# Performance work log

Hardware: AMD Instinct MI355X
Metric: run time of the kernel (lower is better)

The kernel has to match this reference:

```python
import jax, jax.numpy as jnp
import numpy as np

B, N, C_IN, C_H, C_OUT, R, X_DIM = 32, 256, 64, 128, 128, 5, 1024
NEG = -9e15

def _leaky(x, s=0.2):
    return jnp.where(x >= 0, x, s * x)

def gat_layer(atoms, mask, W, b, a):
    # atoms: (B,n,c_in), mask: (B,n,n,R) bool, W: (c_in, R*c), b: (R*c,), a: (R, 2c)
    bs, n, _ = atoms.shape
    c = a.shape[1] // 2
    h = (atoms @ W + b).reshape(bs, n, R, c)            # (B,n,R,c)
    src = jnp.einsum('bnrc,rc->bnr', h, a[:, :c])       # a . h_i part
    dst = jnp.einsum('bnrc,rc->bnr', h, a[:, c:])       # a . h_j part
    logits = _leaky(src[:, :, None, :] + dst[:, None, :, :])  # (B,i,j,R)
    masked = jnp.where(mask, logits, NEG)
    probs = jax.nn.softmax(masked.reshape(bs, n, n * R), axis=2).reshape(bs, n, n, R)
    return jnp.einsum('bijr,bjrc->bic', probs, h)       # (B,n,c)

def setup_inputs() -> dict:
    key = jax.random.key(0)
    ks = jax.random.split(key, 16)
    def p(k, shape, fan):
        return jax.random.normal(k, shape, jnp.float32) * (1.414 / np.sqrt(fan))
    inp = {
        'x': jax.random.normal(ks[0], (B, X_DIM), jnp.float32),
        'y_atoms': jax.random.normal(ks[1], (B, N, C_IN), jnp.float32),
        'y_bonds': jax.random.randint(ks[2], (B, N, N, R), 0, 2, jnp.int32),
        'W1': p(ks[3], (C_IN, R * C_H), C_IN), 'b1': jnp.zeros((R * C_H,), jnp.float32),
        'a1': p(ks[4], (R, 2 * C_H), 2 * C_H),
        'W2': p(ks[5], (C_H, R * C_H), C_H), 'b2': jnp.zeros((R * C_H,), jnp.float32),
        'a2': p(ks[6], (R, 2 * C_H), 2 * C_H),
        'W3': p(ks[7], (C_H, R * C_OUT), C_H), 'b3': jnp.zeros((R * C_OUT,), jnp.float32),
        'a3': p(ks[8], (R, 2 * C_OUT), 2 * C_OUT),
        'We1': p(ks[9], (2 * C_OUT + X_DIM, 256), 2 * C_OUT + X_DIM), 'be1': jnp.zeros((256,), jnp.float32),
        'We2': p(ks[10], (256, 32), 256), 'be2': jnp.zeros((32,), jnp.float32),
        'We3': p(ks[11], (32, 1), 32), 'be3': jnp.zeros((1,), jnp.float32),
    }
    return inp

def reference(x, y_atoms, y_bonds, W1, b1, a1, W2, b2, a2, W3, b3, a3,
              We1, be1, We2, be2, We3, be3):
    mask = (y_bonds == 1)
    h = gat_layer(y_atoms, mask, W1, b1, a1)
    h = _leaky(h)                                   # dropout is identity at eval
    h = gat_layer(h, mask, W2, b2, a2)
    h = _leaky(h)
    h = gat_layer(h, mask, W3, b3, a3)
    y_feats = jnp.concatenate([jnp.mean(h, axis=1), jnp.max(h, axis=1)], axis=1)
    z = jnp.concatenate([x, y_feats], axis=1)
    z = _leaky(z @ We1 + be1)
    z = _leaky(z @ We2 + be2)
    return z @ We3 + be3
```

## Files before the change

### kernel.cpp

```cpp
#include <hip/hip_runtime.h>
#include <cstddef>

#define BB 32
#define NN 256
#define RR 5

typedef __attribute__((ext_vector_type(8))) short bf16x8;
typedef __attribute__((ext_vector_type(4))) float f32x4;

__device__ __forceinline__ float lrelu(float x) { return x >= 0.f ? x : 0.2f * x; }
__device__ __forceinline__ unsigned short f2bf(float x) {
    unsigned u = __float_as_uint(x);
    u += 0x7FFFu + ((u >> 16) & 1u);
    return (unsigned short)(u >> 16);
}
__device__ __forceinline__ float bf2f(unsigned short u) {
    return __uint_as_float((unsigned)u << 16);
}

__global__ __launch_bounds__(256) void k_prep(const float* __restrict__ W1,
                                              const float* __restrict__ W2,
                                              const float* __restrict__ W3,
                                              const float* __restrict__ We1,
                                              const int* __restrict__ bonds,
                                              unsigned short* __restrict__ WT1,
                                              unsigned short* __restrict__ WT2,
                                              unsigned short* __restrict__ WT3,
                                              float* __restrict__ We1T,
                                              unsigned char* __restrict__ maskp) {
    __shared__ float Ls[40][256];
    int blk = blockIdx.x;
    int t = threadIdx.x;
    if (blk < 30) {
        int layer = blk / 10, nt = blk % 10;
        const float* W;
        unsigned short* WT;
        int K;
        if (layer == 0)      { W = W1; WT = WT1; K = 64; }
        else if (layer == 1) { W = W2; WT = WT2; K = 128; }
        else                 { W = W3; WT = WT3; K = 128; }
        int n = nt * 64 + (t & 63);
        for (int kg = (int)(t >> 6); kg < K / 8; kg += 4) {
            bf16x8 v;
#pragma unroll
            for (int e = 0; e < 8; ++e) v[e] = (short)f2bf(W[(size_t)(kg * 8 + e) * 640 + n]);
            *(bf16x8*)&WT[(size_t)n * K + kg * 8] = v;
        }
    } else if (blk < 62) {
        int bt = blk - 30;
        for (int kk = 0; kk < 40; ++kk)
            Ls[kk][t] = We1[(size_t)(bt * 40 + kk) * 256 + t];
        __syncthreads();
#pragma unroll
        for (int q = 0; q < 10; ++q) {
            float4 v;
            v.x = Ls[q * 4 + 0][t]; v.y = Ls[q * 4 + 1][t];
            v.z = Ls[q * 4 + 2][t]; v.w = Ls[q * 4 + 3][t];
            *(float4*)&We1T[(size_t)t * 1280 + bt * 40 + q * 4] = v;
        }
    } else {
        int idx = (blk - 62) * 256 + t;
        const int* p = bonds + (size_t)idx * 5;
        unsigned m = 0;
#pragma unroll
        for (int r = 0; r < 5; ++r) m |= (p[r] == 1) ? (1u << r) : 0u;
        maskp[idx] = (unsigned char)m;
    }
}

template <int K, int MODE>
__global__ __launch_bounds__(256) void k_gemm_h(const float* __restrict__ Af32,
                                                const unsigned short* __restrict__ aggPb,
                                                const float* __restrict__ Zpart,
                                                const unsigned short* __restrict__ WTg,
                                                const float* __restrict__ bias,
                                                const float* __restrict__ avec,
                                                float* __restrict__ srcp,
                                                float* __restrict__ dstp,
                                                unsigned short* __restrict__ hTf) {
    const int t = threadIdx.x;
    const int n0 = blockIdx.x * 64, m0 = blockIdx.y * 64;
    const int w = t >> 6, lane = t & 63;
    const int colg = lane & 15, rquad = lane >> 4;
    const int m = m0 + w * 16 + colg;
    const int koff = rquad * 8;

    float zi = 0.f;
    if (MODE == 1) zi = 1.f / (Zpart[m] + Zpart[8192 + m]);

    f32x4 acc[4] = {};
#pragma unroll
    for (int kk = 0; kk < K; kk += 32) {
        bf16x8 af;
        size_t off = (size_t)m * K + kk + koff;
        if (MODE == 1) {
            bf16x8 p0 = *(const bf16x8*)&aggPb[off];
            bf16x8 p1 = *(const bf16x8*)&aggPb[off + 1048576];
#pragma unroll
            for (int e = 0; e < 8; ++e) {
                float v = bf2f((unsigned short)p0[e]) + bf2f((unsigned short)p1[e]);
                af[e] = (short)f2bf(lrelu(v * zi));
            }
        } else {
            float4 q0 = *(const float4*)&Af32[off];
            float4 q1 = *(const float4*)&Af32[off + 4];
            af[0] = (short)f2bf(q0.x); af[1] = (short)f2bf(q0.y);
            af[2] = (short)f2bf(q0.z); af[3] = (short)f2bf(q0.w);
            af[4] = (short)f2bf(q1.x); af[5] = (short)f2bf(q1.y);
            af[6] = (short)f2bf(q1.z); af[7] = (short)f2bf(q1.w);
        }
#pragma unroll
        for (int ct = 0; ct < 4; ++ct) {
            bf16x8 bfv = *(const bf16x8*)&WTg[(size_t)(n0 + ct * 16 + colg) * K + kk + koff];
            acc[ct] = __builtin_amdgcn_mfma_f32_16x16x32_bf16(af, bfv, acc[ct], 0, 0, 0);
        }
    }

    const int r = n0 >> 7, chalf = n0 & 127;
    const int b = m0 >> 8, jb = m0 & 255;
    float val[4][4];
    float ssum[4] = {0.f, 0.f, 0.f, 0.f}, dsum[4] = {0.f, 0.f, 0.f, 0.f};
#pragma unroll
    for (int ct = 0; ct < 4; ++ct) {
        int cg = chalf + ct * 16 + colg;
        float bv = bias[n0 + ct * 16 + colg];
        float asr = avec[r * 256 + cg];
        float ads = avec[r * 256 + 128 + cg];
#pragma unroll
        for (int reg = 0; reg < 4; ++reg) {
            float v = acc[ct][reg] + bv;
            val[ct][reg] = v;
            ssum[reg] += v * asr;
            dsum[reg] += v * ads;
        }
    }
#pragma unroll
    for (int mk = 1; mk < 16; mk <<= 1)
#pragma unroll
        for (int reg = 0; reg < 4; ++reg) {
            ssum[reg] += __shfl_xor(ssum[reg], mk);
            dsum[reg] += __shfl_xor(dsum[reg], mk);
        }
    if (colg == 0) {
        int half = (n0 >> 6) & 1;
#pragma unroll
        for (int reg = 0; reg < 4; ++reg) {
            int row = m0 + w * 16 + rquad * 4 + reg;
            srcp[half * 40960 + row * 5 + r] = ssum[reg];
            dstp[half * 40960 + row * 5 + r] = dsum[reg];
        }
    }
    {
        const int joct = (jb >> 3) + w * 2 + (rquad >> 1);
        const size_t tile = (size_t)((b * 5 + r) * 32 + joct) * 1024;
        const int sub = (rquad & 1) * 4;
#pragma unroll
        for (int ct = 0; ct < 4; ++ct) {
            int c = chalf + ct * 16 + colg;
            uint2 pk;
            pk.x = (unsigned)f2bf(val[ct][0]) | ((unsigned)f2bf(val[ct][1]) << 16);
            pk.y = (unsigned)f2bf(val[ct][2]) | ((unsigned)f2bf(val[ct][3]) << 16);
            *(uint2*)&hTf[tile + (size_t)c * 8 + sub] = pk;
        }
    }
}

__global__ __launch_bounds__(256) void k_agg(const unsigned short* __restrict__ hTf,
                                             const float* __restrict__ srcp,
                                             const float* __restrict__ dstp,
                                             const unsigned char* __restrict__ maskp,
                                             unsigned short* __restrict__ aggPb,
                                             float* __restrict__ Zpart) {
    __shared__ unsigned short Ps[10240];
    __shared__ float Ss[80], Ds2l[640], Zrow[16];
    const int t = threadIdx.x;
    const int js = blockIdx.x, itile = blockIdx.y, b = blockIdx.z;
    const int ib = b * 256 + itile * 16;
    const int w = t >> 6, lane = t & 63;
    const int colg = lane & 15, rquad = lane >> 4;
    const size_t bbase = (size_t)(b * 5) * 32 * 1024;

    if (t < 80) Ss[t] = srcp[(size_t)ib * 5 + t] + srcp[40960 + (size_t)ib * 5 + t];
    if (t >= 80 && t < 96) Zrow[t - 80] = 0.f;
    for (int idx = t; idx < 640; idx += 256) {
        int jl = idx & 127, rr = idx >> 7;
        size_t o = (size_t)(b * 256 + js * 128 + jl) * 5 + rr;
        Ds2l[rr * 128 + jl] = dstp[o] + dstp[40960 + o];
    }

    bf16x8 pre[2][2];
#pragma unroll
    for (int s = 0; s < 2; ++s) {
        const int joct = js * 16 + s * 4 + rquad;
        const size_t tbase = bbase + (size_t)joct * 1024;
#pragma unroll
        for (int ct = 0; ct < 2; ++ct) {
            int c = w * 32 + ct * 16 + colg;
            pre[s][ct] = *(const bf16x8*)&hTf[tbase + (size_t)c * 8];
        }
    }
    __syncthreads();

    {
        const int i = t & 15;
        float esum = 0.f;
#pragma unroll
        for (int it = 0; it < 5; ++it) {
            int p = it * 256 + t;
            int lane8 = p & 63, s = p >> 6;
            int kq = lane8 >> 4;
            int k0 = s * 32 + kq * 8;
            int rr = k0 >> 7, j0l = k0 & 127;
            uint2 mk8 = *(const uint2*)&maskp[((size_t)(ib + i) << 8) + js * 128 + j0l];
            float sv = Ss[i * 5 + rr];
            bf16x8 pv;
#pragma unroll
            for (int e = 0; e < 8; ++e) {
                unsigned mb = ((e < 4 ? (mk8.x >> (8 * e)) : (mk8.y >> (8 * (e - 4)))) >> rr) & 1u;
                float v = lrelu(sv + Ds2l[rr * 128 + j0l + e]);
                float ev = mb ? __expf(v) : 0.f;
                unsigned short q = f2bf(ev);
                pv[e] = (short)q;
                esum += __uint_as_float((unsigned)q << 16);
            }
            *(bf16x8*)&Ps[p * 8] = pv;
        }
        atomicAdd(&Zrow[i], esum);
    }
    __syncthreads();
    if (t < 16) Zpart[(size_t)js * 8192 + ib + t] = Zrow[t];

    f32x4 acc[2] = {};
#pragma unroll
    for (int s = 0; s < 20; ++s) {
        bf16x8 af = *(const bf16x8*)&Ps[(s * 64 + lane) * 8];
        const int rr = s >> 2;
        const int joct = js * 16 + (s & 3) * 4 + rquad;
        const size_t tbase = bbase + (size_t)(rr * 32 + joct) * 1024;
#pragma unroll
        for (int ct = 0; ct < 2; ++ct) {
            bf16x8 bfv;
            if (s < 2) {
                bfv = pre[s][ct];
            } else {
                int c = w * 32 + ct * 16 + colg;
                bfv = *(const bf16x8*)&hTf[tbase + (size_t)c * 8];
            }
            acc[ct] = __builtin_amdgcn_mfma_f32_16x16x32_bf16(af, bfv, acc[ct], 0, 0, 0);
        }
    }
    unsigned short* op = aggPb + (size_t)js * 1048576;
    const int irow = ib + rquad * 4;
#pragma unroll
    for (int ct = 0; ct < 2; ++ct) {
        int c = w * 32 + ct * 16 + colg;
#pragma unroll
        for (int reg = 0; reg < 4; ++reg)
            op[(size_t)(irow + reg) * 128 + c] = f2bf(acc[ct][reg]);
    }
}

__global__ __launch_bounds__(256) void k_pool(const unsigned short* __restrict__ aggPb,
                                              const float* __restrict__ Zpart,
                                              float* __restrict__ poolS,
                                              float* __restrict__ poolM) {
    int nc = blockIdx.x, b = blockIdx.y;
    int t = threadIdx.x;
    int c = t & 127, sub = t >> 7;
    __shared__ float Zl[32];
    __shared__ float Sh[2][128], Mh[2][128];
    if (t < 32) {
        int rowg = b * 256 + nc * 32 + t;
        Zl[t] = 1.f / (Zpart[rowg] + Zpart[8192 + rowg]);
    }
    __syncthreads();
    float sm = 0.f, mx = -3.4e38f;
#pragma unroll
    for (int nn = 0; nn < 16; ++nn) {
        int nl = sub * 16 + nn;
        size_t o = (size_t)(b * 256 + nc * 32 + nl) * 128 + c;
        float v = (bf2f(aggPb[o]) + bf2f(aggPb[o + 1048576])) * Zl[nl];
        sm += v; mx = fmaxf(mx, v);
    }
    Sh[sub][c] = sm; Mh[sub][c] = mx;
    __syncthreads();
    if (t < 128) {
        poolS[(b * 8 + nc) * 128 + t] = Sh[0][t] + Sh[1][t];
        poolM[(b * 8 + nc) * 128 + t] = fmaxf(Mh[0][t], Mh[1][t]);
    }
}

__global__ __launch_bounds__(256) void k_mlp1(const float* __restrict__ x,
                                              const float* __restrict__ poolS,
                                              const float* __restrict__ poolM,
                                              const float* __restrict__ We1T,
                                              const float* __restrict__ be1,
                                              float* __restrict__ z1g) {
    int og = blockIdx.x, b = blockIdx.y;
    int t = threadIdx.x;
    __shared__ float zs[1280];
    for (int i = t; i < 1024; i += 256) zs[i] = x[b * 1024 + i];
    if (t < 128) {
        float s = 0.f;
#pragma unroll
        for (int nc = 0; nc < 8; ++nc) s += poolS[(b * 8 + nc) * 128 + t];
        zs[1024 + t] = s * (1.f / 256.f);
    } else {
        int f = t - 128;
        float mx = -3.4e38f;
#pragma unroll
        for (int nc = 0; nc < 8; ++nc) mx = fmaxf(mx, poolM[(b * 8 + nc) * 128 + f]);
        zs[1152 + f] = mx;
    }
    __syncthreads();
    int w = t >> 6, lane = t & 63;
#pragma unroll
    for (int oo = 0; oo < 4; ++oo) {
        int o = og * 16 + w * 4 + oo;
        float s = 0.f;
#pragma unroll
        for (int i = 0; i < 20; ++i) {
            int k = i * 64 + lane;
            s += zs[k] * We1T[(size_t)o * 1280 + k];
        }
#pragma unroll
        for (int off = 32; off > 0; off >>= 1) s += __shfl_down(s, off);
        if (lane == 0) z1g[b * 256 + o] = lrelu(s + be1[o]);
    }
}

__global__ __launch_bounds__(256) void k_mlp23(const float* __restrict__ z1g,
                                               const float* __restrict__ We2,
                                               const float* __restrict__ be2,
                                               const float* __restrict__ We3,
                                               const float* __restrict__ be3,
                                               float* __restrict__ out) {
    int b = blockIdx.x, t = threadIdx.x;
    __shared__ float zs[256], z2s[32];
    zs[t] = z1g[b * 256 + t];
    __syncthreads();
    if (t < 32) {
        float s2 = be2[t];
        for (int k = 0; k < 256; ++k) s2 += zs[k] * We2[k * 32 + t];
        z2s[t] = lrelu(s2);
    }
    __syncthreads();
    if (t == 0) {
        float s3 = be3[0];
#pragma unroll
        for (int k = 0; k < 32; ++k) s3 += z2s[k] * We3[k];
        out[b] = s3;
    }
}

constexpr size_t O_MASK  = 0;
constexpr size_t O_SRCP  = 2097152;
constexpr size_t O_DSTP  = O_SRCP + 2ull * 40960 * 4;
constexpr size_t O_AGG   = O_DSTP + 2ull * 40960 * 4;
constexpr size_t O_ZP    = O_AGG + 2ull * 1048576 * 2;
constexpr size_t O_HT    = O_ZP + 2ull * 8192 * 4;
constexpr size_t O_WT1   = O_HT + 5242880ull * 2;
constexpr size_t O_WT2   = O_WT1 + 640ull * 64 * 2;
constexpr size_t O_WT3   = O_WT2 + 640ull * 128 * 2;
constexpr size_t O_WE1T  = O_WT3 + 640ull * 128 * 2;
constexpr size_t O_POOLS = O_WE1T + 256ull * 1280 * 4;
constexpr size_t O_POOLM = O_POOLS + 32ull * 8 * 128 * 4;
constexpr size_t O_Z1    = O_POOLM + 32ull * 8 * 128 * 4;

extern "C" void kernel_launch(void* const* d_in, const int* in_sizes, int n_in,
                              void* d_out, int out_size, void* d_ws, size_t ws_size,
                              hipStream_t stream) {
    const float* x       = (const float*)d_in[0];
    const float* y_atoms = (const float*)d_in[1];
    const int*   y_bonds = (const int*)d_in[2];
    const float* W1 = (const float*)d_in[3];
    const float* b1 = (const float*)d_in[4];
    const float* a1 = (const float*)d_in[5];
    const float* W2 = (const float*)d_in[6];
    const float* b2 = (const float*)d_in[7];
    const float* a2 = (const float*)d_in[8];
    const float* W3 = (const float*)d_in[9];
    const float* b3 = (const float*)d_in[10];
    const float* a3 = (const float*)d_in[11];
    const float* We1 = (const float*)d_in[12];
    const float* be1 = (const float*)d_in[13];
    const float* We2 = (const float*)d_in[14];
    const float* be2 = (const float*)d_in[15];
    const float* We3 = (const float*)d_in[16];
    const float* be3 = (const float*)d_in[17];
    float* out = (float*)d_out;

    char* ws = (char*)d_ws;
    unsigned char* maskp = (unsigned char*)(ws + O_MASK);
    float* srcp = (float*)(ws + O_SRCP);
    float* dstp = (float*)(ws + O_DSTP);
    unsigned short* aggPb = (unsigned short*)(ws + O_AGG);
    float* Zpart = (float*)(ws + O_ZP);
    unsigned short* hTf = (unsigned short*)(ws + O_HT);
    unsigned short* WT1 = (unsigned short*)(ws + O_WT1);
    unsigned short* WT2 = (unsigned short*)(ws + O_WT2);
    unsigned short* WT3 = (unsigned short*)(ws + O_WT3);
    float* We1T  = (float*)(ws + O_WE1T);
    float* poolS = (float*)(ws + O_POOLS);
    float* poolM = (float*)(ws + O_POOLM);
    float* z1g   = (float*)(ws + O_Z1);

    dim3 blk(256);

    k_prep<<<8254, blk, 0, stream>>>(W1, W2, W3, We1, y_bonds, WT1, WT2, WT3, We1T, maskp);

    k_gemm_h<64, 0><<<dim3(10, 128), blk, 0, stream>>>(
        y_atoms, nullptr, nullptr, WT1, b1, a1, srcp, dstp, hTf);
    k_agg<<<dim3(2, 16, 32), blk, 0, stream>>>(hTf, srcp, dstp, maskp, aggPb, Zpart);

    k_gemm_h<128, 1><<<dim3(10, 128), blk, 0, stream>>>(
        nullptr, aggPb, Zpart, WT2, b2, a2, srcp, dstp, hTf);
    k_agg<<<dim3(2, 16, 32), blk, 0, stream>>>(hTf, srcp, dstp, maskp, aggPb, Zpart);

    k_gemm_h<128, 1><<<dim3(10, 128), blk, 0, stream>>>(
        nullptr, aggPb, Zpart, WT3, b3, a3, srcp, dstp, hTf);
    k_agg<<<dim3(2, 16, 32), blk, 0, stream>>>(hTf, srcp, dstp, maskp, aggPb, Zpart);

    k_pool<<<dim3(8, 32), blk, 0, stream>>>(aggPb, Zpart, poolS, poolM);
    k_mlp1<<<dim3(16, 32), blk, 0, stream>>>(x, poolS, poolM, We1T, be1, z1g);
    k_mlp23<<<32, blk, 0, stream>>>(z1g, We2, be2, We3, be3, out);
}
```

Before: 214.9 us.

## Merge split-j aggregation into one block per row tile and fuse tail kernels

The aggregation kernel now handles all 256 neighbours in a single 512-thread block instead of splitting j across two blocks. The softmax normalisation and leaky-ReLU therefore happen inside the aggregation, and the next GEMM reads a single bf16 activation directly. Mask packing is vectorised to four atoms per thread, and the We1 transpose is dropped. Pooling and the three MLP layers are fused into one per-batch tail kernel. This removes partial-sum traffic and several launches, but the grid shrinks to 512 blocks and the fused MLP runs on only 32 blocks with uncoalesced-free but serial dot products.

Measured after the change: 264.9 us. +23.3%, slower.

```diff
diff --git a/kernel.cpp b/kernel.cpp
--- a/kernel.cpp
+++ b/kernel.cpp
@@ -21,14 +21,11 @@
 __global__ __launch_bounds__(256) void k_prep(const float* __restrict__ W1,
                                               const float* __restrict__ W2,
                                               const float* __restrict__ W3,
-                                              const float* __restrict__ We1,
                                               const int* __restrict__ bonds,
                                               unsigned short* __restrict__ WT1,
                                               unsigned short* __restrict__ WT2,
                                               unsigned short* __restrict__ WT3,
-                                              float* __restrict__ We1T,
                                               unsigned char* __restrict__ maskp) {
-    __shared__ float Ls[40][256];
     int blk = blockIdx.x;
     int t = threadIdx.x;
     if (blk < 30) {
@@ -46,32 +43,26 @@
             for (int e = 0; e < 8; ++e) v[e] = (short)f2bf(W[(size_t)(kg * 8 + e) * 640 + n]);
             *(bf16x8*)&WT[(size_t)n * K + kg * 8] = v;
         }
-    } else if (blk < 62) {
-        int bt = blk - 30;
-        for (int kk = 0; kk < 40; ++kk)
-            Ls[kk][t] = We1[(size_t)(bt * 40 + kk) * 256 + t];
-        __syncthreads();
-#pragma unroll
-        for (int q = 0; q < 10; ++q) {
-            float4 v;
-            v.x = Ls[q * 4 + 0][t]; v.y = Ls[q * 4 + 1][t];
-            v.z = Ls[q * 4 + 2][t]; v.w = Ls[q * 4 + 3][t];
-            *(float4*)&We1T[(size_t)t * 1280 + bt * 40 + q * 4] = v;
-        }
     } else {
-        int idx = (blk - 62) * 256 + t;
-        const int* p = bonds + (size_t)idx * 5;
+        int gt = (blk - 30) * 256 + t;
+        const int4* p = (const int4*)(bonds + (size_t)gt * 20);
+        int4 q0 = p[0], q1 = p[1], q2 = p[2], q3 = p[3], q4 = p[4];
+        int v[20] = {q0.x, q0.y, q0.z, q0.w, q1.x, q1.y, q1.z, q1.w,
+                     q2.x, q2.y, q2.z, q2.w, q3.x, q3.y, q3.z, q3.w,
+                     q4.x, q4.y, q4.z, q4.w};
         unsigned m = 0;
 #pragma unroll
-        for (int r = 0; r < 5; ++r) m |= (p[r] == 1) ? (1u << r) : 0u;
-        maskp[idx] = (unsigned char)m;
+        for (int k = 0; k < 4; ++k)
+#pragma unroll
+            for (int r = 0; r < 5; ++r)
+                m |= (v[k * 5 + r] == 1) ? (1u << (k * 8 + r)) : 0u;
+        *(unsigned*)&maskp[(size_t)gt * 4] = m;
     }
 }
 
 template <int K, int MODE>
 __global__ __launch_bounds__(256) void k_gemm_h(const float* __restrict__ Af32,
-                                                const unsigned short* __restrict__ aggPb,
-                                                const float* __restrict__ Zpart,
+                                                const unsigned short* __restrict__ Ab,
                                                 const unsigned short* __restrict__ WTg,
                                                 const float* __restrict__ bias,
                                                 const float* __restrict__ avec,
@@ -85,22 +76,13 @@
     const int m = m0 + w * 16 + colg;
     const int koff = rquad * 8;
 
-    float zi = 0.f;
-    if (MODE == 1) zi = 1.f / (Zpart[m] + Zpart[8192 + m]);
-
     f32x4 acc[4] = {};
 #pragma unroll
     for (int kk = 0; kk < K; kk += 32) {
         bf16x8 af;
         size_t off = (size_t)m * K + kk + koff;
         if (MODE == 1) {
-            bf16x8 p0 = *(const bf16x8*)&aggPb[off];
-            bf16x8 p1 = *(const bf16x8*)&aggPb[off + 1048576];
-#pragma unroll
-            for (int e = 0; e < 8; ++e) {
-                float v = bf2f((unsigned short)p0[e]) + bf2f((unsigned short)p1[e]);
-                af[e] = (short)f2bf(lrelu(v * zi));
-            }
+            af = *(const bf16x8*)&Ab[off];
         } else {
             float4 q0 = *(const float4*)&Af32[off];
             float4 q1 = *(const float4*)&Af32[off + 4];
@@ -165,207 +147,163 @@
     }
 }
 
-__global__ __launch_bounds__(256) void k_agg(const unsigned short* __restrict__ hTf,
-                                             const float* __restrict__ srcp,
-                                             const float* __restrict__ dstp,
-                                             const unsigned char* __restrict__ maskp,
-                                             unsigned short* __restrict__ aggPb,
-                                             float* __restrict__ Zpart) {
-    __shared__ unsigned short Ps[10240];
-    __shared__ float Ss[80], Ds2l[640], Zrow[16];
+template <int FINAL>
+__global__ __launch_bounds__(512, 4) void k_agg(const unsigned short* __restrict__ hTf,
+                                                const float* __restrict__ srcp,
+                                                const float* __restrict__ dstp,
+                                                const unsigned char* __restrict__ maskp,
+                                                unsigned short* __restrict__ Ab,
+                                                float* __restrict__ Ab32) {
+    __shared__ __align__(16) unsigned short Ps[20480];
+    __shared__ __align__(16) float Ds2l[1280];
+    __shared__ float Ss[80], Zw[128], Zrow[16];
     const int t = threadIdx.x;
-    const int js = blockIdx.x, itile = blockIdx.y, b = blockIdx.z;
+    const int itile = blockIdx.x, b = blockIdx.y;
     const int ib = b * 256 + itile * 16;
     const int w = t >> 6, lane = t & 63;
     const int colg = lane & 15, rquad = lane >> 4;
+    const int c = w * 16 + colg;
     const size_t bbase = (size_t)(b * 5) * 32 * 1024;
 
     if (t < 80) Ss[t] = srcp[(size_t)ib * 5 + t] + srcp[40960 + (size_t)ib * 5 + t];
-    if (t >= 80 && t < 96) Zrow[t - 80] = 0.f;
-    for (int idx = t; idx < 640; idx += 256) {
-        int jl = idx & 127, rr = idx >> 7;
-        size_t o = (size_t)(b * 256 + js * 128 + jl) * 5 + rr;
-        Ds2l[rr * 128 + jl] = dstp[o] + dstp[40960 + o];
-    }
-
-    bf16x8 pre[2][2];
-#pragma unroll
-    for (int s = 0; s < 2; ++s) {
-        const int joct = js * 16 + s * 4 + rquad;
-        const size_t tbase = bbase + (size_t)joct * 1024;
-#pragma unroll
-        for (int ct = 0; ct < 2; ++ct) {
-            int c = w * 32 + ct * 16 + colg;
-            pre[s][ct] = *(const bf16x8*)&hTf[tbase + (size_t)c * 8];
-        }
-    }
+    for (int idx = t; idx < 1280; idx += 512) {
+        int jl = idx & 255, rr = idx >> 8;
+        size_t o = (size_t)(b * 256 + jl) * 5 + rr;
+        Ds2l[rr * 256 + jl] = dstp[o] + dstp[40960 + o];
+    }
+    bf16x8 pre[4];
+#pragma unroll
+    for (int s = 0; s < 4; ++s)
+        pre[s] = *(const bf16x8*)&hTf[bbase + (size_t)(s * 4 + rquad) * 1024 + (size_t)c * 8];
     __syncthreads();
 
     {
         const int i = t & 15;
+        const int kq = (t >> 4) & 3;
         float esum = 0.f;
 #pragma unroll
         for (int it = 0; it < 5; ++it) {
-            int p = it * 256 + t;
-            int lane8 = p & 63, s = p >> 6;
-            int kq = lane8 >> 4;
+            int p = it * 512 + t;
+            int s = p >> 6;
             int k0 = s * 32 + kq * 8;
-            int rr = k0 >> 7, j0l = k0 & 127;
-            uint2 mk8 = *(const uint2*)&maskp[((size_t)(ib + i) << 8) + js * 128 + j0l];
+            int rr = k0 >> 8, j0 = k0 & 255;
+            uint2 mk8 = *(const uint2*)&maskp[((size_t)(ib + i) << 8) + j0];
             float sv = Ss[i * 5 + rr];
+            float4 d0 = *(const float4*)&Ds2l[rr * 256 + j0];
+            float4 d1 = *(const float4*)&Ds2l[rr * 256 + j0 + 4];
+            float dv[8] = {d0.x, d0.y, d0.z, d0.w, d1.x, d1.y, d1.z, d1.w};
             bf16x8 pv;
 #pragma unroll
             for (int e = 0; e < 8; ++e) {
                 unsigned mb = ((e < 4 ? (mk8.x >> (8 * e)) : (mk8.y >> (8 * (e - 4)))) >> rr) & 1u;
-                float v = lrelu(sv + Ds2l[rr * 128 + j0l + e]);
-                float ev = mb ? __expf(v) : 0.f;
+                float vv = lrelu(sv + dv[e]);
+                float ev = mb ? __expf(vv) : 0.f;
                 unsigned short q = f2bf(ev);
                 pv[e] = (short)q;
                 esum += __uint_as_float((unsigned)q << 16);
             }
             *(bf16x8*)&Ps[p * 8] = pv;
         }
-        atomicAdd(&Zrow[i], esum);
-    }
-    __syncthreads();
-    if (t < 16) Zpart[(size_t)js * 8192 + ib + t] = Zrow[t];
-
-    f32x4 acc[2] = {};
-#pragma unroll
-    for (int s = 0; s < 20; ++s) {
+        esum += __shfl_xor(esum, 16);
+        esum += __shfl_xor(esum, 32);
+        if (lane < 16) Zw[w * 16 + (lane & 15)] = esum;
+    }
+    __syncthreads();
+    if (t < 16) {
+        float z = 0.f;
+#pragma unroll
+        for (int ww = 0; ww < 8; ++ww) z += Zw[ww * 16 + t];
+        Zrow[t] = 1.f / z;
+    }
+
+    f32x4 acc0 = {}, acc1 = {};
+#pragma unroll
+    for (int s = 0; s < 8; ++s) {
         bf16x8 af = *(const bf16x8*)&Ps[(s * 64 + lane) * 8];
-        const int rr = s >> 2;
-        const int joct = js * 16 + (s & 3) * 4 + rquad;
-        const size_t tbase = bbase + (size_t)(rr * 32 + joct) * 1024;
-#pragma unroll
-        for (int ct = 0; ct < 2; ++ct) {
-            bf16x8 bfv;
-            if (s < 2) {
-                bfv = pre[s][ct];
-            } else {
-                int c = w * 32 + ct * 16 + colg;
-                bfv = *(const bf16x8*)&hTf[tbase + (size_t)c * 8];
-            }
-            acc[ct] = __builtin_amdgcn_mfma_f32_16x16x32_bf16(af, bfv, acc[ct], 0, 0, 0);
-        }
-    }
-    unsigned short* op = aggPb + (size_t)js * 1048576;
+        bf16x8 bfv;
+        if (s < 4) bfv = pre[s];
+        else bfv = *(const bf16x8*)&hTf[bbase + (size_t)((s & 7) * 4 + rquad) * 1024 + (size_t)c * 8];
+        if (s & 1) acc1 = __builtin_amdgcn_mfma_f32_16x16x32_bf16(af, bfv, acc1, 0, 0, 0);
+        else       acc0 = __builtin_amdgcn_mfma_f32_16x16x32_bf16(af, bfv, acc0, 0, 0, 0);
+    }
+#pragma unroll 8
+    for (int s = 8; s < 40; ++s) {
+        bf16x8 af = *(const bf16x8*)&Ps[(s * 64 + lane) * 8];
+        bf16x8 bfv = *(const bf16x8*)&hTf[bbase +
+            (size_t)((s >> 3) * 32 + (s & 7) * 4 + rquad) * 1024 + (size_t)c * 8];
+        if (s & 1) acc1 = __builtin_amdgcn_mfma_f32_16x16x32_bf16(af, bfv, acc1, 0, 0, 0);
+        else       acc0 = __builtin_amdgcn_mfma_f32_16x16x32_bf16(af, bfv, acc0, 0, 0, 0);
+    }
+    __syncthreads();
     const int irow = ib + rquad * 4;
 #pragma unroll
-    for (int ct = 0; ct < 2; ++ct) {
-        int c = w * 32 + ct * 16 + colg;
-#pragma unroll
-        for (int reg = 0; reg < 4; ++reg)
-            op[(size_t)(irow + reg) * 128 + c] = f2bf(acc[ct][reg]);
-    }
-}
-
-__global__ __launch_bounds__(256) void k_pool(const unsigned short* __restrict__ aggPb,
-                                              const float* __restrict__ Zpart,
-                                              float* __restrict__ poolS,
-                                              float* __restrict__ poolM) {
-    int nc = blockIdx.x, b = blockIdx.y;
-    int t = threadIdx.x;
-    int c = t & 127, sub = t >> 7;
-    __shared__ float Zl[32];
+    for (int reg = 0; reg < 4; ++reg) {
+        float v = (acc0[reg] + acc1[reg]) * Zrow[rquad * 4 + reg];
+        if (FINAL) Ab32[(size_t)(irow + reg) * 128 + c] = v;
+        else       Ab[(size_t)(irow + reg) * 128 + c] = f2bf(lrelu(v));
+    }
+}
+
+__global__ __launch_bounds__(256) void k_tail(const float* __restrict__ h3,
+                                              const float* __restrict__ x,
+                                              const float* __restrict__ We1,
+                                              const float* __restrict__ be1,
+                                              const float* __restrict__ We2,
+                                              const float* __restrict__ be2,
+                                              const float* __restrict__ We3,
+                                              const float* __restrict__ be3,
+                                              float* __restrict__ out) {
+    __shared__ float zs[1280];
     __shared__ float Sh[2][128], Mh[2][128];
+    __shared__ float z1s[256], z2s[32];
+    const int b = blockIdx.x, t = threadIdx.x;
+    const int cc = t & 127, sub = t >> 7;
+    float sm = 0.f, mx = -3.4e38f;
+    for (int nn = 0; nn < 128; ++nn) {
+        float v = h3[(size_t)(b * 256 + sub * 128 + nn) * 128 + cc];
+        sm += v;
+        mx = fmaxf(mx, v);
+    }
+    Sh[sub][cc] = sm;
+    Mh[sub][cc] = mx;
+    for (int i = t; i < 1024; i += 256) zs[i] = x[(size_t)b * 1024 + i];
+    __syncthreads();
+    if (t < 128) zs[1024 + t] = (Sh[0][t] + Sh[1][t]) * (1.f / 256.f);
+    else {
+        int f = t - 128;
+        zs[1152 + f] = fmaxf(Mh[0][f], Mh[1][f]);
+    }
+    __syncthreads();
+    {
+        float s = 0.f;
+#pragma unroll 8
+        for (int k = 0; k < 1280; ++k) s += zs[k] * We1[(size_t)k * 256 + t];
+        z1s[t] = lrelu(s + be1[t]);
+    }
+    __syncthreads();
     if (t < 32) {
-        int rowg = b * 256 + nc * 32 + t;
-        Zl[t] = 1.f / (Zpart[rowg] + Zpart[8192 + rowg]);
-    }
-    __syncthreads();
-    float sm = 0.f, mx = -3.4e38f;
-#pragma unroll
-    for (int nn = 0; nn < 16; ++nn) {
-        int nl = sub * 16 + nn;
-        size_t o = (size_t)(b * 256 + nc * 32 + nl) * 128 + c;
-        float v = (bf2f(aggPb[o]) + bf2f(aggPb[o + 1048576])) * Zl[nl];
-        sm += v; mx = fmaxf(mx, v);
-    }
-    Sh[sub][c] = sm; Mh[sub][c] = mx;
-    __syncthreads();
-    if (t < 128) {
-        poolS[(b * 8 + nc) * 128 + t] = Sh[0][t] + Sh[1][t];
-        poolM[(b * 8 + nc) * 128 + t] = fmaxf(Mh[0][t], Mh[1][t]);
-    }
-}
-
-__global__ __launch_bounds__(256) void k_mlp1(const float* __restrict__ x,
-                                              const float* __restrict__ poolS,
-                                              const float* __restrict__ poolM,
-                                              const float* __restrict__ We1T,
-                                              const float* __restrict__ be1,
-                                              float* __restrict__ z1g) {
-    int og = blockIdx.x, b = blockIdx.y;
-    int t = threadIdx.x;
-    __shared__ float zs[1280];
-    for (int i = t; i < 1024; i += 256) zs[i] = x[b * 1024 + i];
-    if (t < 128) {
-        float s = 0.f;
-#pragma unroll
-        for (int nc = 0; nc < 8; ++nc) s += poolS[(b * 8 + nc) * 128 + t];
-        zs[1024 + t] = s * (1.f / 256.f);
-    } else {
-        int f = t - 128;
-        float mx = -3.4e38f;
-#pragma unroll
-        for (int nc = 0; nc < 8; ++nc) mx = fmaxf(mx, poolM[(b * 8 + nc) * 128 + f]);
-        zs[1152 + f] = mx;
-    }
-    __syncthreads();
-    int w = t >> 6, lane = t & 63;
-#pragma unroll
-    for (int oo = 0; oo < 4; ++oo) {
-        int o = og * 16 + w * 4 + oo;
-        float s = 0.f;
-#pragma unroll
-        for (int i = 0; i < 20; ++i) {
-            int k = i * 64 + lane;
-            s += zs[k] * We1T[(size_t)o * 1280 + k];
-        }
-#pragma unroll
-        for (int off = 32; off > 0; off >>= 1) s += __shfl_down(s, off);
-        if (lane == 0) z1g[b * 256 + o] = lrelu(s + be1[o]);
-    }
-}
-
-__global__ __launch_bounds__(256) void k_mlp23(const float* __restrict__ z1g,
-                                               const float* __restrict__ We2,
-                                               const float* __restrict__ be2,
-                                               const float* __restrict__ We3,
-                                               const float* __restrict__ be3,
-                                               float* __restrict__ out) {
-    int b = blockIdx.x, t = threadIdx.x;
-    __shared__ float zs[256], z2s[32];
-    zs[t] = z1g[b * 256 + t];
-    __syncthreads();
-    if (t < 32) {
-        float s2 = be2[t];
-        for (int k = 0; k < 256; ++k) s2 += zs[k] * We2[k * 32 + t];
-        z2s[t] = lrelu(s2);
+        float s2 = 0.f;
+        for (int k = 0; k < 256; ++k) s2 += z1s[k] * We2[k * 32 + t];
+        z2s[t] = lrelu(s2 + be2[t]);
     }
     __syncthreads();
     if (t == 0) {
-        float s3 = be3[0];
+        float s3 = 0.f;
 #pragma unroll
         for (int k = 0; k < 32; ++k) s3 += z2s[k] * We3[k];
-        out[b] = s3;
-    }
-}
-
-constexpr size_t O_MASK  = 0;
-constexpr size_t O_SRCP  = 2097152;
-constexpr size_t O_DSTP  = O_SRCP + 2ull * 40960 * 4;
-constexpr size_t O_AGG   = O_DSTP + 2ull * 40960 * 4;
-constexpr size_t O_ZP    = O_AGG + 2ull * 1048576 * 2;
-constexpr size_t O_HT    = O_ZP + 2ull * 8192 * 4;
-constexpr size_t O_WT1   = O_HT + 5242880ull * 2;
-constexpr size_t O_WT2   = O_WT1 + 640ull * 64 * 2;
-constexpr size_t O_WT3   = O_WT2 + 640ull * 128 * 2;
-constexpr size_t O_WE1T  = O_WT3 + 640ull * 128 * 2;
-constexpr size_t O_POOLS = O_WE1T + 256ull * 1280 * 4;
-constexpr size_t O_POOLM = O_POOLS + 32ull * 8 * 128 * 4;
-constexpr size_t O_Z1    = O_POOLM + 32ull * 8 * 128 * 4;
+        out[b] = s3 + be3[0];
+    }
+}
+
+constexpr size_t O_MASK = 0;
+constexpr size_t O_SRCP = 2097152;
+constexpr size_t O_DSTP = O_SRCP + 2ull * 40960 * 4;
+constexpr size_t O_AB   = O_DSTP + 2ull * 40960 * 4;
+constexpr size_t O_AB32 = O_AB + 2097152;
+constexpr size_t O_HT   = O_AB32 + 4194304;
+constexpr size_t O_WT1  = O_HT + 5242880ull * 2;
+constexpr size_t O_WT2  = O_WT1 + 640ull * 64 * 2;
+constexpr size_t O_WT3  = O_WT2 + 640ull * 128 * 2;
 
 extern "C" void kernel_launch(void* const* d_in, const int* in_sizes, int n_in,
                               void* d_out, int out_size, void* d_ws, size_t ws_size,
@@ -394,34 +332,28 @@
     unsigned char* maskp = (unsigned char*)(ws + O_MASK);
     float* srcp = (float*)(ws + O_SRCP);
     float* dstp = (float*)(ws + O_DSTP);
-    unsigned short* aggPb = (unsigned short*)(ws + O_AGG);
-    float* Zpart = (float*)(ws + O_ZP);
+    unsigned short* Ab = (unsigned short*)(ws + O_AB);
+    float* Ab32 = (float*)(ws + O_AB32);
     unsigned short* hTf = (unsigned short*)(ws + O_HT);
     unsigned short* WT1 = (unsigned short*)(ws + O_WT1);
     unsigned short* WT2 = (unsigned short*)(ws + O_WT2);
     unsigned short* WT3 = (unsigned short*)(ws + O_WT3);
-    float* We1T  = (float*)(ws + O_WE1T);
-    float* poolS = (float*)(ws + O_POOLS);
-    float* poolM = (float*)(ws + O_POOLM);
-    float* z1g   = (float*)(ws + O_Z1);
 
     dim3 blk(256);
 
-    k_prep<<<8254, blk, 0, stream>>>(W1, W2, W3, We1, y_bonds, WT1, WT2, WT3, We1T, maskp);
+    k_prep<<<2078, blk, 0, stream>>>(W1, W2, W3, y_bonds, WT1, WT2, WT3, maskp);
 
     k_gemm_h<64, 0><<<dim3(10, 128), blk, 0, stream>>>(
-        y_atoms, nullptr, nullptr, WT1, b1, a1, srcp, dstp, hTf);
-    k_agg<<<dim3(2, 16, 32), blk, 0, stream>>>(hTf, srcp, dstp, maskp, aggPb, Zpart);
+        y_atoms, nullptr, WT1, b1, a1, srcp, dstp, hTf);
+    k_agg<0><<<dim3(16, 32), dim3(512), 0, stream>>>(hTf, srcp, dstp, maskp, Ab, nullptr);
 
     k_gemm_h<128, 1><<<dim3(10, 128), blk, 0, stream>>>(
-        nullptr, aggPb, Zpart, WT2, b2, a2, srcp, dstp, hTf);
-    k_agg<<<dim3(2, 16, 32), blk, 0, stream>>>(hTf, srcp, dstp, maskp, aggPb, Zpart);
+        nullptr, Ab, WT2, b2, a2, srcp, dstp, hTf);
+    k_agg<0><<<dim3(16, 32), dim3(512), 0, stream>>>(hTf, srcp, dstp, maskp, Ab, nullptr);
 
     k_gemm_h<128, 1><<<dim3(10, 128), blk, 0, stream>>>(
-        nullptr, aggPb, Zpart, WT3, b3, a3, srcp, dstp, hTf);
-    k_agg<<<dim3(2, 16, 32), blk, 0, stream>>>(hTf, srcp, dstp, maskp, aggPb, Zpart);
-
-    k_pool<<<dim3(8, 32), blk, 0, stream>>>(aggPb, Zpart, poolS, poolM);
-    k_mlp1<<<dim3(16, 32), blk, 0, stream>>>(x, poolS, poolM, We1T, be1, z1g);
-    k_mlp23<<<32, blk, 0, stream>>>(z1g, We2, be2, We3, be3, out);
-}
+        nullptr, Ab, WT3, b3, a3, srcp, dstp, hTf);
+    k_agg<1><<<dim3(16, 32), dim3(512), 0, stream>>>(hTf, srcp, dstp, maskp, nullptr, Ab32);
+
+    k_tail<<<32, blk, 0, stream>>>(Ab32, x, We1, be1, We2, be2, We3, be3, out);
+}
```
